# Kernel tuning notes

Hardware: AMD Instinct MI355X
Metric: run time of the kernel (lower is better)

The kernel has to match this reference:

```python
import jax, jax.numpy as jnp
import numpy as np

N, E, IN_F, EDGE_F, HID, S = 200000, 600000, 28, 4, 128, 20000
NUM_LAYERS = 4
L = NUM_LAYERS - 1
BN_EPS = 1e-5


def setup_inputs() -> dict:
    key = jax.random.key(0)
    ks = jax.random.split(key, 20)
    p = lambda k, shape: (jax.random.normal(k, shape, dtype=jnp.float32) * 0.1)
    return {
        'x': jax.random.normal(ks[0], (N, IN_F), dtype=jnp.float32),
        'edge_index': jax.random.randint(ks[1], (2, E), 0, N),
        'edge_attr': jax.random.normal(ks[2], (E, EDGE_F), dtype=jnp.float32),
        'edge_weight': jax.random.uniform(ks[3], (E,), dtype=jnp.float32),
        'node_mask': (jax.random.uniform(ks[4], (N,)) > 0.5).astype(jnp.float32),
        'subgraphs2nodes': jax.random.randint(ks[5], (N,), 0, S),
        # layer-1 params (in_features -> hidden)
        'be1_W1': p(ks[6], (EDGE_F, IN_F)), 'be1_b1': jnp.zeros((IN_F,), jnp.float32),
        'be1_W2': p(ks[7], (IN_F, IN_F)), 'be1_b2': jnp.zeros((IN_F,), jnp.float32),
        'm1_W1': p(ks[8], (IN_F, HID)), 'm1_b1': jnp.zeros((HID,), jnp.float32),
        'm1_W2': p(ks[9], (HID, HID)), 'm1_b2': jnp.zeros((HID,), jnp.float32),
        'bn1_g': jnp.ones((HID,), jnp.float32), 'bn1_b': jnp.zeros((HID,), jnp.float32),
        'eps1': jnp.zeros((), jnp.float32),
        # layers 2..NUM_LAYERS, stacked (hidden -> hidden)
        'beW1': p(ks[10], (L, EDGE_F, HID)), 'beb1': jnp.zeros((L, HID), jnp.float32),
        'beW2': p(ks[11], (L, HID, HID)), 'beb2': jnp.zeros((L, HID), jnp.float32),
        'mW1': p(ks[12], (L, HID, HID)), 'mb1': jnp.zeros((L, HID), jnp.float32),
        'mW2': p(ks[13], (L, HID, HID)), 'mb2': jnp.zeros((L, HID), jnp.float32),
        'bng': jnp.ones((L, HID), jnp.float32), 'bnb': jnp.zeros((L, HID), jnp.float32),
        'eps': jnp.zeros((L,), jnp.float32),
    }


def _mlp2(h, W1, b1, W2, b2):
    # Linear -> ReLU -> Linear
    return jnp.dot(jax.nn.relu(jnp.dot(h, W1) + b1), W2) + b2


def _gine(x, src, dst, edge_attr, edge_weight, eps,
          beW1, beb1, beW2, beb2, W1, b1, W2, b2, g, beta):
    # bond encoder on edge features
    e = _mlp2(edge_attr, beW1, beb1, beW2, beb2)            # [E, d]
    # message: relu(x_j + e_ij) * w_ij, aggregated at dst via scatter-add
    m = jax.nn.relu(x[src] + e) * edge_weight[:, None]      # [E, d]
    aggr = jax.ops.segment_sum(m, dst, num_segments=N)      # [N, d]
    h = (1.0 + eps) * x + aggr
    # node MLP: Linear,ReLU,Linear,BN(train mode),ReLU
    h = _mlp2(h, W1, b1, W2, b2)
    mu = jnp.mean(h, axis=0)
    var = jnp.mean((h - mu) ** 2, axis=0)
    h = (h - mu) * jax.lax.rsqrt(var + BN_EPS) * g + beta
    return jax.nn.relu(h)


def reference(x, edge_index, edge_attr, edge_weight, node_mask, subgraphs2nodes,
              be1_W1, be1_b1, be1_W2, be1_b2, m1_W1, m1_b1, m1_W2, m1_b2,
              bn1_g, bn1_b, eps1,
              beW1, beb1, beW2, beb2, mW1, mb1, mW2, mb2, bng, bnb, eps):
    src, dst = edge_index[0], edge_index[1]
    h = _gine(x, src, dst, edge_attr, edge_weight, eps1,
              be1_W1, be1_b1, be1_W2, be1_b2,
              m1_W1, m1_b1, m1_W2, m1_b2, bn1_g, bn1_b)
    for i in range(L):
        h_new = _gine(h, src, dst, edge_attr, edge_weight, eps[i],
                      beW1[i], beb1[i], beW2[i], beb2[i],
                      mW1[i], mb1[i], mW2[i], mb2[i], bng[i], bnb[i])
        h = h + h_new  # residual
    # float node_mask branch + global_add_pool over subgraphs2nodes
    h = h * node_mask[:, None]
    return jax.ops.segment_sum(h, subgraphs2nodes, num_segments=S)  # [S, HID]
```

## Files before the change

kernel.cpp:

```cpp
#include <hip/hip_runtime.h>
#include <hip/hip_bf16.h>


#define BNEPS 1e-5f
#define LDA 136
#define SCAN_NB 240

typedef __attribute__((ext_vector_type(8))) short bf16x8;
typedef __attribute__((ext_vector_type(8))) unsigned short u16x8;
typedef __attribute__((ext_vector_type(4))) float f32x4;

__device__ inline short f2bf(float f) {
    __hip_bfloat16 h = __float2bfloat16(f);
    return *reinterpret_cast<short*>(&h);
}
__device__ inline unsigned short f2bfu(float f) {
    __hip_bfloat16 h = __float2bfloat16(f);
    return *reinterpret_cast<unsigned short*>(&h);
}
__device__ inline float bf2f(unsigned short u) {
    union { unsigned int i; float f; } v; v.i = ((unsigned int)u) << 16; return v.f;
}

__global__ __launch_bounds__(256) void k_prep(
    const float* __restrict__ m1W2, const float* __restrict__ beW2,
    const float* __restrict__ mW1, const float* __restrict__ mW2,
    short* __restrict__ out)
{
    __shared__ float tileS[64][65];
    int b = blockIdx.x, mat = b >> 2, t = b & 3;
    const float* Wsrc;
    if (mat == 0) Wsrc = m1W2;
    else {
        int l = (mat - 1) / 3, which = (mat - 1) % 3;
        Wsrc = (which == 0) ? beW2 + (size_t)l * 16384
             : (which == 1) ? mW1 + (size_t)l * 16384
             :                mW2 + (size_t)l * 16384;
    }
    short* dst = out + (size_t)mat * 16384;
    int tr = (t >> 1) * 64, tc = (t & 1) * 64;
    for (int i = threadIdx.x; i < 4096; i += 256) {
        int r = i >> 6, c = i & 63;
        tileS[r][c] = Wsrc[(size_t)(tr + r) * 128 + (tc + c)];
    }
    __syncthreads();
    for (int i = threadIdx.x; i < 4096; i += 256) {
        int n = i >> 6, k = i & 63;
        dst[(size_t)(tc + n) * 128 + (tr + k)] = f2bf(tileS[k][n]);
    }
}

__global__ __launch_bounds__(256) void k_prep1(
    const float* __restrict__ W1, short* __restrict__ out)
{
    for (int i = threadIdx.x; i < 128 * 32; i += 256) {
        int n = i >> 5, k = i & 31;
        out[i] = (k < 28) ? f2bf(W1[(size_t)k * 128 + n]) : (short)0;
    }
}

__global__ __launch_bounds__(256) void k_count(
    const int* __restrict__ ei, int* __restrict__ counts, int E)
{
    for (int e = blockIdx.x * 256 + threadIdx.x; e < E; e += gridDim.x * 256)
        atomicAdd(&counts[ei[E + e]], 1);
}

__global__ __launch_bounds__(256) void k_count2(
    const int* __restrict__ s2n, const float* __restrict__ mask,
    int* __restrict__ counts2, int N)
{
    for (int n = blockIdx.x * 256 + threadIdx.x; n < N; n += gridDim.x * 256)
        if (mask[n] != 0.f) atomicAdd(&counts2[s2n[n]], 1);
}

__global__ __launch_bounds__(256) void k_scanA(
    const int* __restrict__ counts, int* __restrict__ bsum, int N, int seg)
{
    __shared__ int red[256];
    int b = blockIdx.x;
    int lo = b * seg, hi = min(lo + seg, N);
    int s = 0;
    for (int i = lo + threadIdx.x; i < hi; i += 256) s += counts[i];
    red[threadIdx.x] = s;
    __syncthreads();
    for (int d = 128; d > 0; d >>= 1) {
        if (threadIdx.x < d) red[threadIdx.x] += red[threadIdx.x + d];
        __syncthreads();
    }
    if (threadIdx.x == 0) bsum[b] = red[0];
}

__global__ __launch_bounds__(256) void k_scanB(
    int* __restrict__ bsum, int nb, int* __restrict__ offs, int N)
{
    __shared__ int sh[256];
    int v = (threadIdx.x < nb) ? bsum[threadIdx.x] : 0;
    sh[threadIdx.x] = v;
    __syncthreads();
    for (int d = 1; d < 256; d <<= 1) {
        int t = (threadIdx.x >= d) ? sh[threadIdx.x - d] : 0;
        __syncthreads();
        sh[threadIdx.x] += t;
        __syncthreads();
    }
    if (threadIdx.x < nb) bsum[threadIdx.x] = sh[threadIdx.x] - v;
    if (threadIdx.x == 0) offs[N] = sh[255];
}

__global__ __launch_bounds__(256) void k_scanC(
    const int* __restrict__ counts, const int* __restrict__ bsum,
    int* __restrict__ offs, int* __restrict__ cursor, int N, int seg)
{
    __shared__ int sh[256];
    int b = blockIdx.x;
    int lo = b * seg, hi = min(lo + seg, N);
    int base = bsum[b];
    for (int t0 = lo; t0 < hi; t0 += 256) {
        int i = t0 + threadIdx.x;
        int v = (i < hi) ? counts[i] : 0;
        sh[threadIdx.x] = v;
        __syncthreads();
        for (int d = 1; d < 256; d <<= 1) {
            int t = (threadIdx.x >= d) ? sh[threadIdx.x - d] : 0;
            __syncthreads();
            sh[threadIdx.x] += t;
            __syncthreads();
        }
        int excl = base + sh[threadIdx.x] - v;
        if (i < hi) { offs[i] = excl; cursor[i] = excl; }
        int tileTotal = sh[255];
        __syncthreads();
        base += tileTotal;
    }
}

__global__ __launch_bounds__(256) void k_scatter(
    const int* __restrict__ ei, const float* __restrict__ ew,
    int* __restrict__ cursor, int* __restrict__ perm, int2* __restrict__ pmeta, int E)
{
    for (int e = blockIdx.x * 256 + threadIdx.x; e < E; e += gridDim.x * 256) {
        int d = ei[E + e];
        int pos = atomicAdd(&cursor[d], 1);
        perm[pos] = e;
        pmeta[pos] = make_int2(ei[e], __float_as_int(ew[e]));
    }
}

__global__ __launch_bounds__(256) void k_scatter2(
    const int* __restrict__ s2n, const float* __restrict__ mask,
    int* __restrict__ cursor2, int* __restrict__ perm2, int N)
{
    for (int n = blockIdx.x * 256 + threadIdx.x; n < N; n += gridDim.x * 256)
        if (mask[n] != 0.f) {
            int pos = atomicAdd(&cursor2[s2n[n]], 1);
            perm2[pos] = n;
        }
}

__global__ __launch_bounds__(256) void k_emsg(
    const int* __restrict__ perm, const float4* __restrict__ ea4,
    const float* __restrict__ W1, const float* __restrict__ b1,
    const short* __restrict__ W2t, const float* __restrict__ b2,
    unsigned short* __restrict__ emsg, int e0, int e1)
{
    __shared__ short Bs[128 * LDA];
    __shared__ short As[64 * LDA];
    __shared__ float eas[64][4];
    int tid = threadIdx.x;
    for (int i = tid; i < 2048; i += 256) {
        int n = (i * 8) >> 7, k = (i * 8) & 127;
        *(bf16x8*)&Bs[n * LDA + k] = *(const bf16x8*)&W2t[i * 8];
    }
    int j = tid & 127, half = tid >> 7;
    float w10 = W1[j], w11 = W1[128 + j], w12 = W1[256 + j], w13 = W1[384 + j];
    float b1j = b1[j];
    int w = tid >> 6, lane = tid & 63;
    int l15 = lane & 15, quad = lane >> 4;
    __syncthreads();

    int numTiles = (e1 - e0 + 63) >> 6;
    for (int tile = blockIdx.x; tile < numTiles; tile += gridDim.x) {
        int base = e0 + tile * 64;
        __syncthreads();
        if (tid < 64) {
            int k = base + tid;
            float4 a = make_float4(0.f, 0.f, 0.f, 0.f);
            if (k < e1) a = ea4[perm[k]];
            eas[tid][0] = a.x; eas[tid][1] = a.y; eas[tid][2] = a.z; eas[tid][3] = a.w;
        }
        __syncthreads();
        #pragma unroll
        for (int q = 0; q < 32; ++q) {
            int e = half * 32 + q;
            float t = fmaf(eas[e][0], w10, fmaf(eas[e][1], w11,
                      fmaf(eas[e][2], w12, fmaf(eas[e][3], w13, b1j))));
            As[e * LDA + j] = f2bf(fmaxf(t, 0.f));
        }
        __syncthreads();
        f32x4 acc[8];
        #pragma unroll
        for (int nt = 0; nt < 8; ++nt) acc[nt] = (f32x4){0.f, 0.f, 0.f, 0.f};
        #pragma unroll
        for (int kt = 0; kt < 4; ++kt) {
            bf16x8 af = *(bf16x8*)&As[(w * 16 + l15) * LDA + kt * 32 + quad * 8];
            #pragma unroll
            for (int nt = 0; nt < 8; ++nt) {
                bf16x8 bf = *(bf16x8*)&Bs[(nt * 16 + l15) * LDA + kt * 32 + quad * 8];
                acc[nt] = __builtin_amdgcn_mfma_f32_16x16x32_bf16(af, bf, acc[nt], 0, 0, 0);
            }
        }
        #pragma unroll
        for (int nt = 0; nt < 8; ++nt) {
            int col = nt * 16 + l15;
            float b2c = b2[col];
            #pragma unroll
            for (int r = 0; r < 4; ++r) {
                int row = w * 16 + quad * 4 + r;
                As[row * LDA + col] = f2bf(acc[nt][r] + b2c);
            }
        }
        __syncthreads();
        #pragma unroll
        for (int kk = 0; kk < 4; ++kk) {
            int i = tid + kk * 256;
            int row = (i * 8) >> 7, col = (i * 8) & 127;
            int gr = base + row;
            if (gr < e1)
                *(bf16x8*)&emsg[(size_t)(gr - e0) * 128 + col] = *(bf16x8*)&As[row * LDA + col];
        }
    }
}

__global__ __launch_bounds__(256) void k_gather(
    const unsigned short* __restrict__ h, const int* __restrict__ offs,
    const int2* __restrict__ pmeta, const unsigned short* __restrict__ emsg,
    unsigned short* __restrict__ a0,
    const float* __restrict__ epsp, int epsIdx, int init,
    int e0, int e1, int N)
{
    int grp = threadIdx.x >> 5, lane = threadIdx.x & 31;
    int n = blockIdx.x * 8 + grp;
    if (n >= N) return;
    int k0 = offs[n], k1 = offs[n + 1];
    int lo = max(k0, e0), hi = min(k1, e1);
    if (!init && lo >= hi) return;
    float m0 = 0.f, m1 = 0.f, m2 = 0.f, m3 = 0.f;
    for (int k = lo; k < hi; ++k) {
        int2 mt = pmeta[k];
        float w = __int_as_float(mt.y);
        ushort4 ev = *(const ushort4*)&emsg[(size_t)(k - e0) * 128 + lane * 4];
        ushort4 hv = *(const ushort4*)&h[(size_t)mt.x * 128 + lane * 4];
        m0 += fmaxf(bf2f(hv.x) + bf2f(ev.x), 0.f) * w;
        m1 += fmaxf(bf2f(hv.y) + bf2f(ev.y), 0.f) * w;
        m2 += fmaxf(bf2f(hv.z) + bf2f(ev.z), 0.f) * w;
        m3 += fmaxf(bf2f(hv.w) + bf2f(ev.w), 0.f) * w;
    }
    if (init) {
        float s = 1.0f + epsp[epsIdx];
        ushort4 hv = *(const ushort4*)&h[(size_t)n * 128 + lane * 4];
        m0 = fmaf(s, bf2f(hv.x), m0);
        m1 = fmaf(s, bf2f(hv.y), m1);
        m2 = fmaf(s, bf2f(hv.z), m2);
        m3 = fmaf(s, bf2f(hv.w), m3);
    } else {
        ushort4 cur = *(ushort4*)&a0[(size_t)n * 128 + lane * 4];
        m0 += bf2f(cur.x); m1 += bf2f(cur.y); m2 += bf2f(cur.z); m3 += bf2f(cur.w);
    }
    ushort4 o;
    o.x = f2bfu(m0); o.y = f2bfu(m1); o.z = f2bfu(m2); o.w = f2bfu(m3);
    *(ushort4*)&a0[(size_t)n * 128 + lane * 4] = o;
}

__global__ __launch_bounds__(256) void k_emsg28(
    const int* __restrict__ perm, const float4* __restrict__ ea4,
    const float* __restrict__ W1, const float* __restrict__ b1,
    const float* __restrict__ W2, const float* __restrict__ b2,
    unsigned short* __restrict__ emsg28, int E)
{
    __shared__ float W1s[4*28], W2s[28*28], b1s[28], b2s[28];
    __shared__ float tbuf[8][28];
    int tid = threadIdx.x;
    for (int i = tid; i < 4*28; i += 256) W1s[i] = W1[i];
    for (int i = tid; i < 28*28; i += 256) W2s[i] = W2[i];
    if (tid < 28) { b1s[tid] = b1[tid]; b2s[tid] = b2[tid]; }
    __syncthreads();
    int sub = tid >> 5, j = tid & 31;
    int numGroups = (E + 7) >> 3;
    for (int gb = blockIdx.x; gb < numGroups; gb += gridDim.x) {
        int k = gb * 8 + sub;
        bool valid = (k < E);
        float4 a = valid ? ea4[perm[k]] : make_float4(0.f, 0.f, 0.f, 0.f);
        if (j < 28) {
            float t = a.x*W1s[j] + a.y*W1s[28+j] + a.z*W1s[56+j] + a.w*W1s[84+j] + b1s[j];
            tbuf[sub][j] = fmaxf(t, 0.f);
        }
        __syncthreads();
        if (valid && j < 28) {
            float acc = b2s[j];
            #pragma unroll
            for (int i = 0; i < 28; ++i) acc = fmaf(tbuf[sub][i], W2s[i*28 + j], acc);
            emsg28[(size_t)k * 28 + j] = f2bfu(acc);
        }
        __syncthreads();
    }
}

__global__ __launch_bounds__(256) void k_gather28(
    const float* __restrict__ x, const int* __restrict__ offs,
    const int2* __restrict__ pmeta, const unsigned short* __restrict__ emsg28,
    const float* __restrict__ eps1, float* __restrict__ u28, int N)
{
    int grp = threadIdx.x >> 5, lane = threadIdx.x & 31;
    int n = blockIdx.x * 8 + grp;
    if (n >= N || lane >= 28) return;
    float s = 1.0f + eps1[0];
    int k0 = offs[n], k1 = offs[n + 1];
    float m = 0.f;
    for (int k = k0; k < k1; ++k) {
        int2 mt = pmeta[k];
        float w = __int_as_float(mt.y);
        float e = bf2f(emsg28[(size_t)k * 28 + lane]);
        m += fmaxf(x[(size_t)mt.x * 28 + lane] + e, 0.f) * w;
    }
    u28[(size_t)n * 28 + lane] = fmaf(s, x[(size_t)n * 28 + lane], m);
}

__global__ __launch_bounds__(512) void k_mlp(
    const unsigned short* __restrict__ src, const short* __restrict__ Wt1,
    const float* __restrict__ b1, const short* __restrict__ Wt2,
    const float* __restrict__ b2, unsigned short* __restrict__ dst,
    float* __restrict__ stats, int N)
{
    __shared__ short Bs1[128 * LDA];
    __shared__ short Bs2[128 * LDA];
    __shared__ short As[128 * LDA];
    __shared__ float sstat[256];
    int tid = threadIdx.x;
    for (int i = tid; i < 2048; i += 512) {
        int n = (i * 8) >> 7, k = (i * 8) & 127;
        *(bf16x8*)&Bs1[n * LDA + k] = *(const bf16x8*)&Wt1[i * 8];
        *(bf16x8*)&Bs2[n * LDA + k] = *(const bf16x8*)&Wt2[i * 8];
    }
    if (tid < 256) sstat[tid] = 0.f;
    int w = tid >> 6, lane = tid & 63;
    int l15 = lane & 15, quad = lane >> 4;
    float b1r[8], b2r[8], lsum[8], lsq[8];
    #pragma unroll
    for (int nt = 0; nt < 8; ++nt) {
        int col = nt * 16 + l15;
        b1r[nt] = b1[col]; b2r[nt] = b2[col];
        lsum[nt] = 0.f; lsq[nt] = 0.f;
    }
    __syncthreads();

    int numTiles = (N + 127) >> 7;
    for (int tile = blockIdx.x; tile < numTiles; tile += gridDim.x) {
        int base = tile * 128;
        __syncthreads();
        #pragma unroll
        for (int kk = 0; kk < 4; ++kk) {
            int i = tid + kk * 512;
            int row = (i * 8) >> 7, col = (i * 8) & 127;
            int rr = base + row;
            bf16x8 v;
            if (rr < N) v = *(const bf16x8*)&src[(size_t)rr * 128 + col];
            else        v = (bf16x8){0,0,0,0,0,0,0,0};
            *(bf16x8*)&As[row * LDA + col] = v;
        }
        __syncthreads();
        f32x4 acc[8];
        #pragma unroll
        for (int nt = 0; nt < 8; ++nt) acc[nt] = (f32x4){0.f, 0.f, 0.f, 0.f};
        #pragma unroll
        for (int kt = 0; kt < 4; ++kt) {
            bf16x8 af = *(bf16x8*)&As[(w * 16 + l15) * LDA + kt * 32 + quad * 8];
            #pragma unroll
            for (int nt = 0; nt < 8; ++nt) {
                bf16x8 bf = *(bf16x8*)&Bs1[(nt * 16 + l15) * LDA + kt * 32 + quad * 8];
                acc[nt] = __builtin_amdgcn_mfma_f32_16x16x32_bf16(af, bf, acc[nt], 0, 0, 0);
            }
        }
        #pragma unroll
        for (int nt = 0; nt < 8; ++nt) {
            int col = nt * 16 + l15;
            #pragma unroll
            for (int r = 0; r < 4; ++r)
                As[(w * 16 + quad * 4 + r) * LDA + col] = f2bf(fmaxf(acc[nt][r] + b1r[nt], 0.f));
        }
        __syncthreads();
        #pragma unroll
        for (int nt = 0; nt < 8; ++nt) acc[nt] = (f32x4){0.f, 0.f, 0.f, 0.f};
        #pragma unroll
        for (int kt = 0; kt < 4; ++kt) {
            bf16x8 af = *(bf16x8*)&As[(w * 16 + l15) * LDA + kt * 32 + quad * 8];
            #pragma unroll
            for (int nt = 0; nt < 8; ++nt) {
                bf16x8 bf = *(bf16x8*)&Bs2[(nt * 16 + l15) * LDA + kt * 32 + quad * 8];
                acc[nt] = __builtin_amdgcn_mfma_f32_16x16x32_bf16(af, bf, acc[nt], 0, 0, 0);
            }
        }
        int row0 = base + w * 16 + quad * 4;
        #pragma unroll
        for (int nt = 0; nt < 8; ++nt) {
            int col = nt * 16 + l15;
            #pragma unroll
            for (int r = 0; r < 4; ++r) {
                float z = acc[nt][r] + b2r[nt];
                if (row0 + r < N) { lsum[nt] += z; lsq[nt] = fmaf(z, z, lsq[nt]); }
                As[(w * 16 + quad * 4 + r) * LDA + col] = f2bf(z);
            }
        }
        __syncthreads();
        #pragma unroll
        for (int kk = 0; kk < 4; ++kk) {
            int i = tid + kk * 512;
            int row = (i * 8) >> 7, col = (i * 8) & 127;
            int rr = base + row;
            if (rr < N)
                *(bf16x8*)&dst[(size_t)rr * 128 + col] = *(bf16x8*)&As[row * LDA + col];
        }
    }
    #pragma unroll
    for (int nt = 0; nt < 8; ++nt) {
        int col = nt * 16 + l15;
        atomicAdd(&sstat[col], lsum[nt]);
        atomicAdd(&sstat[128 + col], lsq[nt]);
    }
    __syncthreads();
    if (tid < 256) atomicAdd(&stats[tid], sstat[tid]);
}

__global__ __launch_bounds__(512) void k_mlp1(
    const float* __restrict__ u28, const short* __restrict__ Wt1p,
    const float* __restrict__ b1, const short* __restrict__ Wt2,
    const float* __restrict__ b2, unsigned short* __restrict__ dst,
    float* __restrict__ stats, int N)
{
    __shared__ short Bs1[128 * 40];
    __shared__ short Bs2[128 * LDA];
    __shared__ short As[128 * LDA];
    __shared__ short A28[128 * 40];
    __shared__ float sstat[256];
    int tid = threadIdx.x;
    for (int i = tid; i < 128 * 32; i += 512) {
        int n = i >> 5, k = i & 31;
        Bs1[n * 40 + k] = Wt1p[i];
    }
    for (int i = tid; i < 2048; i += 512) {
        int n = (i * 8) >> 7, k = (i * 8) & 127;
        *(bf16x8*)&Bs2[n * LDA + k] = *(const bf16x8*)&Wt2[i * 8];
    }
    {
        int r = tid >> 2, c = tid & 3;
        if (tid < 512) A28[r * 40 + 28 + c] = 0;
    }
    if (tid < 256) sstat[tid] = 0.f;
    int w = tid >> 6, lane = tid & 63;
    int l15 = lane & 15, quad = lane >> 4;
    float b1r[8], b2r[8], lsum[8], lsq[8];
    #pragma unroll
    for (int nt = 0; nt < 8; ++nt) {
        int col = nt * 16 + l15;
        b1r[nt] = b1[col]; b2r[nt] = b2[col];
        lsum[nt] = 0.f; lsq[nt] = 0.f;
    }
    __syncthreads();

    int numTiles = (N + 127) >> 7;
    for (int tile = blockIdx.x; tile < numTiles; tile += gridDim.x) {
        int base = tile * 128;
        __syncthreads();
        for (int i = tid; i < 128 * 28; i += 512) {
            int row = i / 28, col = i - row * 28;
            int rr = base + row;
            A28[row * 40 + col] = (rr < N) ? f2bf(u28[(size_t)rr * 28 + col]) : (short)0;
        }
        __syncthreads();
        f32x4 acc[8];
        #pragma unroll
        for (int nt = 0; nt < 8; ++nt) acc[nt] = (f32x4){0.f, 0.f, 0.f, 0.f};
        {
            bf16x8 af = *(bf16x8*)&A28[(w * 16 + l15) * 40 + quad * 8];
            #pragma unroll
            for (int nt = 0; nt < 8; ++nt) {
                bf16x8 bf = *(bf16x8*)&Bs1[(nt * 16 + l15) * 40 + quad * 8];
                acc[nt] = __builtin_amdgcn_mfma_f32_16x16x32_bf16(af, bf, acc[nt], 0, 0, 0);
            }
        }
        #pragma unroll
        for (int nt = 0; nt < 8; ++nt) {
            int col = nt * 16 + l15;
            #pragma unroll
            for (int r = 0; r < 4; ++r)
                As[(w * 16 + quad * 4 + r) * LDA + col] = f2bf(fmaxf(acc[nt][r] + b1r[nt], 0.f));
        }
        __syncthreads();
        #pragma unroll
        for (int nt = 0; nt < 8; ++nt) acc[nt] = (f32x4){0.f, 0.f, 0.f, 0.f};
        #pragma unroll
        for (int kt = 0; kt < 4; ++kt) {
            bf16x8 af = *(bf16x8*)&As[(w * 16 + l15) * LDA + kt * 32 + quad * 8];
            #pragma unroll
            for (int nt = 0; nt < 8; ++nt) {
                bf16x8 bf = *(bf16x8*)&Bs2[(nt * 16 + l15) * LDA + kt * 32 + quad * 8];
                acc[nt] = __builtin_amdgcn_mfma_f32_16x16x32_bf16(af, bf, acc[nt], 0, 0, 0);
            }
        }
        int row0 = base + w * 16 + quad * 4;
        #pragma unroll
        for (int nt = 0; nt < 8; ++nt) {
            int col = nt * 16 + l15;
            #pragma unroll
            for (int r = 0; r < 4; ++r) {
                float z = acc[nt][r] + b2r[nt];
                if (row0 + r < N) { lsum[nt] += z; lsq[nt] = fmaf(z, z, lsq[nt]); }
                As[(w * 16 + quad * 4 + r) * LDA + col] = f2bf(z);
            }
        }
        __syncthreads();
        #pragma unroll
        for (int kk = 0; kk < 4; ++kk) {
            int i = tid + kk * 512;
            int row = (i * 8) >> 7, col = (i * 8) & 127;
            int rr = base + row;
            if (rr < N)
                *(bf16x8*)&dst[(size_t)rr * 128 + col] = *(bf16x8*)&As[row * LDA + col];
        }
    }
    #pragma unroll
    for (int nt = 0; nt < 8; ++nt) {
        int col = nt * 16 + l15;
        atomicAdd(&sstat[col], lsum[nt]);
        atomicAdd(&sstat[128 + col], lsq[nt]);
    }
    __syncthreads();
    if (tid < 256) atomicAdd(&stats[tid], sstat[tid]);
}

__global__ __launch_bounds__(128) void k_stats(
    const float* __restrict__ stats, const float* __restrict__ g,
    const float* __restrict__ b, float* __restrict__ ss, float invN)
{
    int j = threadIdx.x;
    float mu  = stats[j] * invN;
    float var = fmaf(stats[128 + j], invN, -mu * mu);
    float sc  = rsqrtf(fmaxf(var, 0.f) + BNEPS) * g[j];
    ss[j] = sc;
    ss[128 + j] = fmaf(-mu, sc, b[j]);
}

__global__ __launch_bounds__(256) void k_bn(
    const unsigned short* __restrict__ z, const float* __restrict__ ss,
    unsigned short* __restrict__ h, int residual, int N)
{
    int idx8 = blockIdx.x * 256 + threadIdx.x;
    int stride = gridDim.x * 256;
    int c0 = (idx8 & 15) * 8;
    float scl[8], sht[8];
    #pragma unroll
    for (int r = 0; r < 8; ++r) { scl[r] = ss[c0 + r]; sht[r] = ss[128 + c0 + r]; }
    int total8 = N * 16;
    for (; idx8 < total8; idx8 += stride) {
        int n = idx8 >> 4;
        u16x8 z8 = *(const u16x8*)&z[(size_t)n * 128 + c0];
        float hn[8];
        #pragma unroll
        for (int r = 0; r < 8; ++r)
            hn[r] = fmaxf(fmaf(bf2f(z8[r]), scl[r], sht[r]), 0.f);
        if (residual) {
            u16x8 h8 = *(const u16x8*)&h[(size_t)n * 128 + c0];
            #pragma unroll
            for (int r = 0; r < 8; ++r) hn[r] += bf2f(h8[r]);
        }
        u16x8 o;
        #pragma unroll
        for (int r = 0; r < 8; ++r) o[r] = f2bfu(hn[r]);
        *(u16x8*)&h[(size_t)n * 128 + c0] = o;
    }
}

__global__ __launch_bounds__(256) void k_pool(
    const unsigned short* __restrict__ h, const int* __restrict__ offs2,
    const int* __restrict__ perm2, float* __restrict__ out, int S)
{
    int w = threadIdx.x >> 6, lane = threadIdx.x & 63;
    int s = blockIdx.x * 4 + w;
    if (s >= S) return;
    int k0 = offs2[s], k1 = offs2[s + 1];
    float a0 = 0.f, a1 = 0.f;
    for (int k = k0; k < k1; ++k) {
        int n = perm2[k];
        ushort2 hv = *(const ushort2*)&h[(size_t)n * 128 + lane * 2];
        a0 += bf2f(hv.x); a1 += bf2f(hv.y);
    }
    *(float2*)&out[(size_t)s * 128 + lane * 2] = make_float2(a0, a1);
}

extern "C" void kernel_launch(void* const* d_in, const int* in_sizes, int n_in,
                              void* d_out, int out_size, void* d_ws, size_t ws_size,
                              hipStream_t stream) {
    const float* x    = (const float*)d_in[0];
    const int*   ei   = (const int*)d_in[1];
    const float* ea   = (const float*)d_in[2];
    const float* ew   = (const float*)d_in[3];
    const float* mask = (const float*)d_in[4];
    const int*   s2n  = (const int*)d_in[5];
    const float* be1W1 = (const float*)d_in[6];
    const float* be1b1 = (const float*)d_in[7];
    const float* be1W2 = (const float*)d_in[8];
    const float* be1b2 = (const float*)d_in[9];
    const float* m1W1  = (const float*)d_in[10];
    const float* m1b1  = (const float*)d_in[11];
    const float* m1W2  = (const float*)d_in[12];
    const float* m1b2  = (const float*)d_in[13];
    const float* bn1g  = (const float*)d_in[14];
    const float* bn1b  = (const float*)d_in[15];
    const float* eps1  = (const float*)d_in[16];
    const float* beW1  = (const float*)d_in[17];
    const float* beb1  = (const float*)d_in[18];
    const float* beW2  = (const float*)d_in[19];
    const float* beb2  = (const float*)d_in[20];
    const float* mW1   = (const float*)d_in[21];
    const float* mb1   = (const float*)d_in[22];
    const float* mW2   = (const float*)d_in[23];
    const float* mb2   = (const float*)d_in[24];
    const float* bng   = (const float*)d_in[25];
    const float* bnb   = (const float*)d_in[26];
    const float* epsL  = (const float*)d_in[27];

    const int N = in_sizes[0] / 28;
    const int E = in_sizes[1] / 2;
    const int S = out_size / 128;
    const float invN = 1.0f / (float)N;
    const int EC = (E + 1) / 2;

    auto al16 = [](size_t v) { return (v + 15) & ~(size_t)15; };
    char* ws = (char*)d_ws;
    size_t offH      = 0;
    size_t offA0     = al16(offH + (size_t)N * 256);
    size_t offEm     = al16(offA0 + (size_t)N * 256);
    size_t emBytes   = (size_t)EC * 256;
    if ((size_t)E * 56 > emBytes) emBytes = (size_t)E * 56;
    size_t offStats  = al16(offEm + emBytes);
    size_t offSS     = al16(offStats + 4096);
    size_t offWts    = al16(offSS + 1024);
    size_t offCounts = al16(offWts + 10 * 16384 * 2 + 4096 * 2);
    size_t offOffs   = al16(offCounts + (size_t)N * 4);
    size_t offCursor = al16(offOffs + (size_t)(N + 1) * 4);
    size_t offPerm   = al16(offCursor + (size_t)N * 4);
    size_t offPmeta  = al16(offPerm + (size_t)E * 4);
    size_t offBsum   = al16(offPmeta + (size_t)E * 8);
    size_t offCnt2   = al16(offBsum + SCAN_NB * 4);
    size_t offOffs2  = al16(offCnt2 + (size_t)S * 4);
    size_t offCur2   = al16(offOffs2 + (size_t)(S + 1) * 4);
    size_t offPerm2  = al16(offCur2 + (size_t)S * 4);
    size_t need      = offPerm2 + (size_t)N * 4;
    if (ws_size < need) return;

    unsigned short* h    = (unsigned short*)(ws + offH);
    unsigned short* a0   = (unsigned short*)(ws + offA0);
    unsigned short* emsg = (unsigned short*)(ws + offEm);
    float* u28    = (float*)(ws + offA0);
    float* stats  = (float*)(ws + offStats);
    float* ssbuf  = (float*)(ws + offSS);
    short* wts    = (short*)(ws + offWts);
    short* w1p    = wts + 10 * 16384;
    int*   counts = (int*)(ws + offCounts);
    int*   offs   = (int*)(ws + offOffs);
    int*   cursor = (int*)(ws + offCursor);
    int*   perm   = (int*)(ws + offPerm);
    int2*  pmeta  = (int2*)(ws + offPmeta);
    int*   bsum   = (int*)(ws + offBsum);
    int*   cnt2   = (int*)(ws + offCnt2);
    int*   offs2  = (int*)(ws + offOffs2);
    int*   cur2   = (int*)(ws + offCur2);
    int*   perm2  = (int*)(ws + offPerm2);
    const float4* ea4 = (const float4*)ea;

    hipMemsetAsync(stats, 0, 4 * 256 * sizeof(float), stream);
    hipMemsetAsync(counts, 0, (size_t)N * sizeof(int), stream);
    hipMemsetAsync(cnt2, 0, (size_t)S * sizeof(int), stream);

    k_prep<<<40, 256, 0, stream>>>(m1W2, beW2, mW1, mW2, wts);
    k_prep1<<<1, 256, 0, stream>>>(m1W1, w1p);

    const int seg = (N + SCAN_NB - 1) / SCAN_NB;
    k_count<<<1024, 256, 0, stream>>>(ei, counts, E);
    k_scanA<<<SCAN_NB, 256, 0, stream>>>(counts, bsum, N, seg);
    k_scanB<<<1, 256, 0, stream>>>(bsum, SCAN_NB, offs, N);
    k_scanC<<<SCAN_NB, 256, 0, stream>>>(counts, bsum, offs, cursor, N, seg);
    k_scatter<<<1024, 256, 0, stream>>>(ei, ew, cursor, perm, pmeta, E);

    const int seg2 = (S + SCAN_NB - 1) / SCAN_NB;
    k_count2<<<512, 256, 0, stream>>>(s2n, mask, cnt2, N);
    k_scanA<<<SCAN_NB, 256, 0, stream>>>(cnt2, bsum, S, seg2);
    k_scanB<<<1, 256, 0, stream>>>(bsum, SCAN_NB, offs2, S);
    k_scanC<<<SCAN_NB, 256, 0, stream>>>(cnt2, bsum, offs2, cur2, S, seg2);
    k_scatter2<<<512, 256, 0, stream>>>(s2n, mask, cur2, perm2, N);

    auto wt_be = [&](int l) { return wts + (size_t)(1 + 3 * l + 0) * 16384; };
    auto wt_m1 = [&](int l) { return wts + (size_t)(1 + 3 * l + 1) * 16384; };
    auto wt_m2 = [&](int l) { return wts + (size_t)(1 + 3 * l + 2) * 16384; };

    int gatherBlocks = (N + 7) / 8;

    k_emsg28<<<2048, 256, 0, stream>>>(perm, ea4, be1W1, be1b1, be1W2, be1b2, emsg, E);
    k_gather28<<<gatherBlocks, 256, 0, stream>>>(x, offs, pmeta, emsg, eps1, u28, N);
    k_mlp1<<<256, 512, 0, stream>>>(u28, w1p, m1b1, wts , m1b2, h, stats, N);
    k_stats<<<1, 128, 0, stream>>>(stats, bn1g, bn1b, ssbuf, invN);
    k_bn<<<2048, 256, 0, stream>>>(h, ssbuf, h, 0, N);

    for (int l = 0; l < 3; ++l) {
        for (int c = 0; c < 2; ++c) {
            int e0 = c * EC, e1 = min(e0 + EC, E);
            k_emsg<<<2048, 256, 0, stream>>>(perm, ea4,
                beW1 + (size_t)l * 512, beb1 + (size_t)l * 128,
                wt_be(l), beb2 + (size_t)l * 128, emsg, e0, e1);
            k_gather<<<gatherBlocks, 256, 0, stream>>>(h, offs, pmeta, emsg, a0,
                epsL, l, (c == 0) ? 1 : 0, e0, e1, N);
        }
        k_mlp<<<256, 512, 0, stream>>>(a0, wt_m1(l), mb1 + (size_t)l * 128,
                                       wt_m2(l), mb2 + (size_t)l * 128, a0,
                                       stats + 256 * (l + 1), N);
        k_stats<<<1, 128, 0, stream>>>(stats + 256 * (l + 1),
            bng + (size_t)l * 128, bnb + (size_t)l * 128, ssbuf, invN);
        k_bn<<<2048, 256, 0, stream>>>(a0, ssbuf, h, 1, N);
    }

    k_pool<<<(S + 3) / 4, 256, 0, stream>>>(h, offs2, perm2, (float*)d_out, S);
}
```

Measured before the change: 1.137 ms.

## Pre-permute edge attributes, MFMA first-layer bond encoder, fuse last BN into pooling

```diff
diff --git a/kernel.cpp b/kernel.cpp
--- a/kernel.cpp
+++ b/kernel.cpp
@@ -59,6 +59,15 @@
     }
 }
 
+__global__ __launch_bounds__(256) void k_prep28(
+    const float* __restrict__ W2, short* __restrict__ out)
+{
+    for (int i = threadIdx.x; i < 32 * 32; i += 256) {
+        int n = i >> 5, k = i & 31;
+        out[i] = (n < 28 && k < 28) ? f2bf(W2[(size_t)k * 28 + n]) : (short)0;
+    }
+}
+
 __global__ __launch_bounds__(256) void k_count(
     const int* __restrict__ ei, int* __restrict__ counts, int E)
 {
@@ -137,13 +146,15 @@
 
 __global__ __launch_bounds__(256) void k_scatter(
     const int* __restrict__ ei, const float* __restrict__ ew,
-    int* __restrict__ cursor, int* __restrict__ perm, int2* __restrict__ pmeta, int E)
+    const float4* __restrict__ ea4,
+    int* __restrict__ cursor, int2* __restrict__ pmeta,
+    float4* __restrict__ pea4, int E)
 {
     for (int e = blockIdx.x * 256 + threadIdx.x; e < E; e += gridDim.x * 256) {
         int d = ei[E + e];
         int pos = atomicAdd(&cursor[d], 1);
-        perm[pos] = e;
         pmeta[pos] = make_int2(ei[e], __float_as_int(ew[e]));
+        pea4[pos] = ea4[e];
     }
 }
 
@@ -159,7 +170,7 @@
 }
 
 __global__ __launch_bounds__(256) void k_emsg(
-    const int* __restrict__ perm, const float4* __restrict__ ea4,
+    const float4* __restrict__ pea4,
     const float* __restrict__ W1, const float* __restrict__ b1,
     const short* __restrict__ W2t, const float* __restrict__ b2,
     unsigned short* __restrict__ emsg, int e0, int e1)
@@ -186,7 +197,7 @@
         if (tid < 64) {
             int k = base + tid;
             float4 a = make_float4(0.f, 0.f, 0.f, 0.f);
-            if (k < e1) a = ea4[perm[k]];
+            if (k < e1) a = pea4[k];
             eas[tid][0] = a.x; eas[tid][1] = a.y; eas[tid][2] = a.z; eas[tid][3] = a.w;
         }
         __syncthreads();
@@ -228,6 +239,75 @@
             int gr = base + row;
             if (gr < e1)
                 *(bf16x8*)&emsg[(size_t)(gr - e0) * 128 + col] = *(bf16x8*)&As[row * LDA + col];
+        }
+    }
+}
+
+__global__ __launch_bounds__(256) void k_emsg28_mm(
+    const float4* __restrict__ pea4,
+    const float* __restrict__ W1, const float* __restrict__ b1,
+    const short* __restrict__ W2t28,
+    const float* __restrict__ b2,
+    unsigned short* __restrict__ emsg28, int E)
+{
+    __shared__ short Bs[32 * 40];
+    __shared__ short As[64 * 40];
+    __shared__ float eas[64][4];
+    __shared__ float b2s[32];
+    int tid = threadIdx.x;
+    for (int i = tid; i < 32 * 32; i += 256) {
+        int n = i >> 5, k = i & 31;
+        Bs[n * 40 + k] = W2t28[i];
+    }
+    if (tid < 32) b2s[tid] = (tid < 28) ? b2[tid] : 0.f;
+    int j = tid & 31, sub = tid >> 5;
+    float w10 = 0.f, w11 = 0.f, w12 = 0.f, w13 = 0.f, b1j = 0.f;
+    if (j < 28) { w10 = W1[j]; w11 = W1[28 + j]; w12 = W1[56 + j]; w13 = W1[84 + j]; b1j = b1[j]; }
+    int w = tid >> 6, lane = tid & 63;
+    int l15 = lane & 15, quad = lane >> 4;
+    __syncthreads();
+
+    int numTiles = (E + 63) >> 6;
+    for (int tile = blockIdx.x; tile < numTiles; tile += gridDim.x) {
+        int base = tile * 64;
+        __syncthreads();
+        if (tid < 64) {
+            int k = base + tid;
+            float4 a = (k < E) ? pea4[k] : make_float4(0.f, 0.f, 0.f, 0.f);
+            eas[tid][0] = a.x; eas[tid][1] = a.y; eas[tid][2] = a.z; eas[tid][3] = a.w;
+        }
+        __syncthreads();
+        #pragma unroll
+        for (int q = 0; q < 8; ++q) {
+            int e = q * 8 + sub;
+            float t = fmaf(eas[e][0], w10, fmaf(eas[e][1], w11,
+                      fmaf(eas[e][2], w12, fmaf(eas[e][3], w13, b1j))));
+            As[e * 40 + j] = (j < 28) ? f2bf(fmaxf(t, 0.f)) : (short)0;
+        }
+        __syncthreads();
+        f32x4 acc[2];
+        acc[0] = (f32x4){0.f, 0.f, 0.f, 0.f};
+        acc[1] = (f32x4){0.f, 0.f, 0.f, 0.f};
+        bf16x8 af = *(bf16x8*)&As[(w * 16 + l15) * 40 + quad * 8];
+        #pragma unroll
+        for (int nt = 0; nt < 2; ++nt) {
+            bf16x8 bf = *(bf16x8*)&Bs[(nt * 16 + l15) * 40 + quad * 8];
+            acc[nt] = __builtin_amdgcn_mfma_f32_16x16x32_bf16(af, bf, acc[nt], 0, 0, 0);
+        }
+        __syncthreads();
+        #pragma unroll
+        for (int nt = 0; nt < 2; ++nt) {
+            int col = nt * 16 + l15;
+            float bb = b2s[col];
+            #pragma unroll
+            for (int r = 0; r < 4; ++r)
+                As[(w * 16 + quad * 4 + r) * 40 + col] = f2bf(acc[nt][r] + bb);
+        }
+        __syncthreads();
+        for (int i = tid; i < 64 * 28; i += 256) {
+            int row = i / 28, col = i - row * 28;
+            int gr = base + row;
+            if (gr < E) emsg28[(size_t)gr * 28 + col] = As[row * 40 + col];
         }
     }
 }
@@ -272,40 +352,6 @@
     *(ushort4*)&a0[(size_t)n * 128 + lane * 4] = o;
 }
 
-__global__ __launch_bounds__(256) void k_emsg28(
-    const int* __restrict__ perm, const float4* __restrict__ ea4,
-    const float* __restrict__ W1, const float* __restrict__ b1,
-    const float* __restrict__ W2, const float* __restrict__ b2,
-    unsigned short* __restrict__ emsg28, int E)
-{
-    __shared__ float W1s[4*28], W2s[28*28], b1s[28], b2s[28];
-    __shared__ float tbuf[8][28];
-    int tid = threadIdx.x;
-    for (int i = tid; i < 4*28; i += 256) W1s[i] = W1[i];
-    for (int i = tid; i < 28*28; i += 256) W2s[i] = W2[i];
-    if (tid < 28) { b1s[tid] = b1[tid]; b2s[tid] = b2[tid]; }
-    __syncthreads();
-    int sub = tid >> 5, j = tid & 31;
-    int numGroups = (E + 7) >> 3;
-    for (int gb = blockIdx.x; gb < numGroups; gb += gridDim.x) {
-        int k = gb * 8 + sub;
-        bool valid = (k < E);
-        float4 a = valid ? ea4[perm[k]] : make_float4(0.f, 0.f, 0.f, 0.f);
-        if (j < 28) {
-            float t = a.x*W1s[j] + a.y*W1s[28+j] + a.z*W1s[56+j] + a.w*W1s[84+j] + b1s[j];
-            tbuf[sub][j] = fmaxf(t, 0.f);
-        }
-        __syncthreads();
-        if (valid && j < 28) {
-            float acc = b2s[j];
-            #pragma unroll
-            for (int i = 0; i < 28; ++i) acc = fmaf(tbuf[sub][i], W2s[i*28 + j], acc);
-            emsg28[(size_t)k * 28 + j] = f2bfu(acc);
-        }
-        __syncthreads();
-    }
-}
-
 __global__ __launch_bounds__(256) void k_gather28(
     const float* __restrict__ x, const int* __restrict__ offs,
     const int2* __restrict__ pmeta, const unsigned short* __restrict__ emsg28,
@@ -580,21 +626,27 @@
     }
 }
 
-__global__ __launch_bounds__(256) void k_pool(
-    const unsigned short* __restrict__ h, const int* __restrict__ offs2,
+__global__ __launch_bounds__(256) void k_poolbn(
+    const unsigned short* __restrict__ z, const unsigned short* __restrict__ hprev,
+    const float* __restrict__ ss, const int* __restrict__ offs2,
     const int* __restrict__ perm2, float* __restrict__ out, int S)
 {
     int w = threadIdx.x >> 6, lane = threadIdx.x & 63;
     int s = blockIdx.x * 4 + w;
     if (s >= S) return;
+    int c0 = lane * 2;
+    float scl0 = ss[c0], scl1 = ss[c0 + 1];
+    float sht0 = ss[128 + c0], sht1 = ss[128 + c0 + 1];
     int k0 = offs2[s], k1 = offs2[s + 1];
     float a0 = 0.f, a1 = 0.f;
     for (int k = k0; k < k1; ++k) {
         int n = perm2[k];
-        ushort2 hv = *(const ushort2*)&h[(size_t)n * 128 + lane * 2];
-        a0 += bf2f(hv.x); a1 += bf2f(hv.y);
-    }
-    *(float2*)&out[(size_t)s * 128 + lane * 2] = make_float2(a0, a1);
+        ushort2 zv = *(const ushort2*)&z[(size_t)n * 128 + c0];
+        ushort2 hv = *(const ushort2*)&hprev[(size_t)n * 128 + c0];
+        a0 += fmaxf(fmaf(bf2f(zv.x), scl0, sht0), 0.f) + bf2f(hv.x);
+        a1 += fmaxf(fmaf(bf2f(zv.y), scl1, sht1), 0.f) + bf2f(hv.y);
+    }
+    *(float2*)&out[(size_t)s * 128 + c0] = make_float2(a0, a1);
 }
 
 extern "C" void kernel_launch(void* const* d_in, const int* in_sizes, int n_in,
@@ -645,12 +697,12 @@
     size_t offStats  = al16(offEm + emBytes);
     size_t offSS     = al16(offStats + 4096);
     size_t offWts    = al16(offSS + 1024);
-    size_t offCounts = al16(offWts + 10 * 16384 * 2 + 4096 * 2);
+    size_t offCounts = al16(offWts + 10 * 16384 * 2 + 4096 * 2 + 1024 * 2);
     size_t offOffs   = al16(offCounts + (size_t)N * 4);
     size_t offCursor = al16(offOffs + (size_t)(N + 1) * 4);
-    size_t offPerm   = al16(offCursor + (size_t)N * 4);
-    size_t offPmeta  = al16(offPerm + (size_t)E * 4);
-    size_t offBsum   = al16(offPmeta + (size_t)E * 8);
+    size_t offPmeta  = al16(offCursor + (size_t)N * 4);
+    size_t offPea    = al16(offPmeta + (size_t)E * 8);
+    size_t offBsum   = al16(offPea + (size_t)E * 16);
     size_t offCnt2   = al16(offBsum + SCAN_NB * 4);
     size_t offOffs2  = al16(offCnt2 + (size_t)S * 4);
     size_t offCur2   = al16(offOffs2 + (size_t)(S + 1) * 4);
@@ -666,11 +718,12 @@
     float* ssbuf  = (float*)(ws + offSS);
     short* wts    = (short*)(ws + offWts);
     short* w1p    = wts + 10 * 16384;
+    short* w2p28  = w1p + 4096;
     int*   counts = (int*)(ws + offCounts);
     int*   offs   = (int*)(ws + offOffs);
     int*   cursor = (int*)(ws + offCursor);
-    int*   perm   = (int*)(ws + offPerm);
     int2*  pmeta  = (int2*)(ws + offPmeta);
+    float4* pea4  = (float4*)(ws + offPea);
     int*   bsum   = (int*)(ws + offBsum);
     int*   cnt2   = (int*)(ws + offCnt2);
     int*   offs2  = (int*)(ws + offOffs2);
@@ -684,13 +737,14 @@
 
     k_prep<<<40, 256, 0, stream>>>(m1W2, beW2, mW1, mW2, wts);
     k_prep1<<<1, 256, 0, stream>>>(m1W1, w1p);
+    k_prep28<<<1, 256, 0, stream>>>(be1W2, w2p28);
 
     const int seg = (N + SCAN_NB - 1) / SCAN_NB;
     k_count<<<1024, 256, 0, stream>>>(ei, counts, E);
     k_scanA<<<SCAN_NB, 256, 0, stream>>>(counts, bsum, N, seg);
     k_scanB<<<1, 256, 0, stream>>>(bsum, SCAN_NB, offs, N);
     k_scanC<<<SCAN_NB, 256, 0, stream>>>(counts, bsum, offs, cursor, N, seg);
-    k_scatter<<<1024, 256, 0, stream>>>(ei, ew, cursor, perm, pmeta, E);
+    k_scatter<<<1024, 256, 0, stream>>>(ei, ew, ea4, cursor, pmeta, pea4, E);
 
     const int seg2 = (S + SCAN_NB - 1) / SCAN_NB;
     k_count2<<<512, 256, 0, stream>>>(s2n, mask, cnt2, N);
@@ -705,7 +759,7 @@
 
     int gatherBlocks = (N + 7) / 8;
 
-    k_emsg28<<<2048, 256, 0, stream>>>(perm, ea4, be1W1, be1b1, be1W2, be1b2, emsg, E);
+    k_emsg28_mm<<<2048, 256, 0, stream>>>(pea4, be1W1, be1b1, w2p28, be1b2, emsg, E);
     k_gather28<<<gatherBlocks, 256, 0, stream>>>(x, offs, pmeta, emsg, eps1, u28, N);
     k_mlp1<<<256, 512, 0, stream>>>(u28, w1p, m1b1, wts , m1b2, h, stats, N);
     k_stats<<<1, 128, 0, stream>>>(stats, bn1g, bn1b, ssbuf, invN);
@@ -714,7 +768,7 @@
     for (int l = 0; l < 3; ++l) {
         for (int c = 0; c < 2; ++c) {
             int e0 = c * EC, e1 = min(e0 + EC, E);
-            k_emsg<<<2048, 256, 0, stream>>>(perm, ea4,
+            k_emsg<<<2048, 256, 0, stream>>>(pea4,
                 beW1 + (size_t)l * 512, beb1 + (size_t)l * 128,
                 wt_be(l), beb2 + (size_t)l * 128, emsg, e0, e1);
             k_gather<<<gatherBlocks, 256, 0, stream>>>(h, offs, pmeta, emsg, a0,
@@ -725,8 +779,11 @@
                                        stats + 256 * (l + 1), N);
         k_stats<<<1, 128, 0, stream>>>(stats + 256 * (l + 1),
             bng + (size_t)l * 128, bnb + (size_t)l * 128, ssbuf, invN);
-        k_bn<<<2048, 256, 0, stream>>>(a0, ssbuf, h, 1, N);
-    }
-
-    k_pool<<<(S + 3) / 4, 256, 0, stream>>>(h, offs2, perm2, (float*)d_out, S);
-}
+        if (l < 2) {
+            k_bn<<<2048, 256, 0, stream>>>(a0, ssbuf, h, 1, N);
+        }
+    }
+
+    k_poolbn<<<(S + 3) / 4, 256, 0, stream>>>(a0, h, ssbuf, offs2, perm2,
+                                              (float*)d_out, S);
+}
```

Result: faster. 1.062 ms (-6.6%).
